# Kernel tuning notes

Hardware: AMD Instinct MI355X
Metric: run time of the kernel (lower is better)

The kernel has to match this reference:

```python
import jax, jax.numpy as jnp
import numpy as np

TOP_K = 3
EPS = 1e-12  # F.normalize eps


def _lstm(x, W_ih, W_hh, b_ih, b_hh):
    # x: [B, S, I]; PyTorch gate order i, f, g, o; returns h sequence [B, S, H]
    B = x.shape[0]
    H = W_hh.shape[1]
    xs = jnp.swapaxes(x, 0, 1)  # [S, B, I]
    x_proj = xs @ W_ih.T + b_ih + b_hh  # [S, B, 4H]

    def step(carry, xp):
        h, c = carry
        gates = xp + h @ W_hh.T
        i, f, g, o = jnp.split(gates, 4, axis=-1)
        i = jax.nn.sigmoid(i); f = jax.nn.sigmoid(f)
        g = jnp.tanh(g); o = jax.nn.sigmoid(o)
        c = f * c + i * g
        h = o * jnp.tanh(c)
        return (h, c), h

    init = (jnp.zeros((B, H), x.dtype), jnp.zeros((B, H), x.dtype))
    _, hs = jax.lax.scan(step, init, x_proj)
    return jnp.swapaxes(hs, 0, 1)  # [B, S, H]


def setup_inputs() -> dict:
    key = jax.random.key(0)
    ks = jax.random.split(key, 16)
    B, S, I, H, M, N, O = 4, 256, 512, 1024, 256, 65536, 512
    sc = 0.02
    return {
        "x": jax.random.normal(ks[0], (B, S, I), jnp.float32),
        "keys": jax.random.normal(ks[1], (N, M), jnp.float32),
        "values": jax.random.normal(ks[2], (N, M), jnp.float32),
        "importance": jnp.ones((N,), jnp.float32),
        "W_ih": jax.random.normal(ks[3], (4 * H, I), jnp.float32) * sc,
        "W_hh": jax.random.normal(ks[4], (4 * H, H), jnp.float32) * sc,
        "b_ih": jnp.zeros((4 * H,), jnp.float32),
        "b_hh": jnp.zeros((4 * H,), jnp.float32),
        "Wq": jax.random.normal(ks[5], (M, H), jnp.float32) * sc,
        "bq": jnp.zeros((M,), jnp.float32),
        "Wa": jax.random.normal(ks[6], (1, M), jnp.float32) * sc,
        "ba": jnp.zeros((1,), jnp.float32),
        "Wc": jax.random.normal(ks[7], (M, M), jnp.float32) * sc,
        "bc": jnp.zeros((M,), jnp.float32),
        "Wo": jax.random.normal(ks[8], (O, H + M), jnp.float32) * sc,
        "bo": jnp.zeros((O,), jnp.float32),
    }


def reference(x, keys, values, importance, W_ih, W_hh, b_ih, b_hh,
              Wq, bq, Wa, ba, Wc, bc, Wo, bo):
    # Controller LSTM over the whole sequence
    h = _lstm(x, W_ih, W_hh, b_ih, b_hh)  # [B, S, H]

    # Query projection and cosine similarity against the memory keys
    q = h @ Wq.T + bq  # [B, S, M]
    qn = q / jnp.maximum(jnp.linalg.norm(q, axis=-1, keepdims=True), EPS)
    kn = keys / jnp.maximum(jnp.linalg.norm(keys, axis=-1, keepdims=True), EPS)
    sim = jnp.einsum("bsm,nm->bsn", qn, kn) * importance  # [B, S, N]

    # Top-k retrieval and value gather
    _, top_idx = jax.lax.top_k(sim, TOP_K)  # [B, S, k]
    retrieved = values[top_idx]  # [B, S, k, M]

    # Learned attention over retrieved memories
    att_logits = (retrieved @ Wa.T + ba)[..., 0]  # [B, S, k]
    att = jax.nn.softmax(att_logits, axis=-1)
    mem = jnp.einsum("bsk,bskm->bsm", att, retrieved)
    mem = mem @ Wc.T + bc  # combine_layer

    out = jnp.concatenate([h, mem], axis=-1) @ Wo.T + bo  # [B, S, O]
    return out
```

## Files before the change

kernel.cpp:

```cpp
#include <hip/hip_runtime.h>
#include <hip/hip_bf16.h>
#include <cstdint>
#include <cstddef>

#define BB 4
#define SS 256
#define ID 512
#define HD 1024
#define MD 256
#define NKEY 65536
#define OD 512
#define ROWS 1024
#define NWG_LSTM 256
#define NTH_LSTM 256
#define KPB 2048
#define KSPLITS (NKEY / KPB)

typedef __attribute__((ext_vector_type(8))) short bf16x8;
typedef __attribute__((ext_vector_type(4))) float f32x4;
typedef __attribute__((ext_vector_type(8))) unsigned short u16x8;

__global__ __launch_bounds__(256) void sgemm_nt(
    const float* __restrict__ A, int lda,
    const float* __restrict__ Bm, int ldb,
    float* __restrict__ C, int ldc, int K,
    const float* __restrict__ bias, const float* __restrict__ bias2,
    int accum)
{
    __shared__ float As[64][17];
    __shared__ float Bs[64][17];
    const int t = threadIdx.x;
    const int tx = t & 15, ty = t >> 4;
    const int bm = blockIdx.y << 6, bn = blockIdx.x << 6;
    const int lrow = t >> 2, lk4 = (t & 3) << 2;
    float acc[4][4] = {};

    for (int kb = 0; kb < K; kb += 16) {
        const float4 av = *(const float4*)&A[(size_t)(bm + lrow) * lda + kb + lk4];
        const float4 bv = *(const float4*)&Bm[(size_t)(bn + lrow) * ldb + kb + lk4];
        __syncthreads();
        As[lrow][lk4 + 0] = av.x; As[lrow][lk4 + 1] = av.y;
        As[lrow][lk4 + 2] = av.z; As[lrow][lk4 + 3] = av.w;
        Bs[lrow][lk4 + 0] = bv.x; Bs[lrow][lk4 + 1] = bv.y;
        Bs[lrow][lk4 + 2] = bv.z; Bs[lrow][lk4 + 3] = bv.w;
        __syncthreads();
#pragma unroll
        for (int k = 0; k < 16; ++k) {
            const float a0 = As[4 * ty + 0][k], a1 = As[4 * ty + 1][k];
            const float a2 = As[4 * ty + 2][k], a3 = As[4 * ty + 3][k];
            const float b0 = Bs[4 * tx + 0][k], b1 = Bs[4 * tx + 1][k];
            const float b2 = Bs[4 * tx + 2][k], b3 = Bs[4 * tx + 3][k];
            acc[0][0] += a0 * b0; acc[0][1] += a0 * b1; acc[0][2] += a0 * b2; acc[0][3] += a0 * b3;
            acc[1][0] += a1 * b0; acc[1][1] += a1 * b1; acc[1][2] += a1 * b2; acc[1][3] += a1 * b3;
            acc[2][0] += a2 * b0; acc[2][1] += a2 * b1; acc[2][2] += a2 * b2; acc[2][3] += a2 * b3;
            acc[3][0] += a3 * b0; acc[3][1] += a3 * b1; acc[3][2] += a3 * b2; acc[3][3] += a3 * b3;
        }
    }

#pragma unroll
    for (int i = 0; i < 4; ++i) {
        const int row = bm + 4 * ty + i;
        const int col = bn + 4 * tx;
        float4* cp = (float4*)&C[(size_t)row * ldc + col];
        float4 r;
        if (accum) {
            const float4 old = *cp;
            r.x = old.x + acc[i][0]; r.y = old.y + acc[i][1];
            r.z = old.z + acc[i][2]; r.w = old.w + acc[i][3];
        } else {
            float bx = bias[col + 0], by = bias[col + 1], bz = bias[col + 2], bw = bias[col + 3];
            if (bias2) { bx += bias2[col + 0]; by += bias2[col + 1]; bz += bias2[col + 2]; bw += bias2[col + 3]; }
            r.x = acc[i][0] + bx; r.y = acc[i][1] + by;
            r.z = acc[i][2] + bz; r.w = acc[i][3] + bw;
        }
        *cp = r;
    }
}

__global__ void rownorm(const float* __restrict__ X, const float* __restrict__ imp,
                        float* __restrict__ scale_out, float* __restrict__ Xn, int nrows)
{
    const int row = blockIdx.x * 4 + (threadIdx.x >> 6);
    const int lane = threadIdx.x & 63;
    if (row >= nrows) return;
    float4 v = *(const float4*)&X[(size_t)row * 256 + (lane << 2)];
    float ss = v.x * v.x + v.y * v.y + v.z * v.z + v.w * v.w;
#pragma unroll
    for (int o = 1; o < 64; o <<= 1) ss += __shfl_xor(ss, o);
    float sc = 1.f / fmaxf(sqrtf(ss), 1e-12f);
    if (imp) sc *= imp[row];
    if (scale_out && lane == 0) scale_out[row] = sc;
    if (Xn) {
        v.x *= sc; v.y *= sc; v.z *= sc; v.w *= sc;
        *(float4*)&Xn[(size_t)row * 256 + (lane << 2)] = v;
    }
}

__device__ inline float sigm_f(float x) { return 1.f / (1.f + __expf(-x)); }
__device__ inline float tanh_f(float x) { return 1.f - 2.f / (__expf(2.f * x) + 1.f); }

#define SUBSTEP(B, U, UN, C4, XPC) do {                                           \
    asm volatile("s_waitcnt vmcnt(3)" ::: "memory");                              \
    __builtin_amdgcn_sched_barrier(0);                                            \
    const unsigned* pb_ = rec + (slot << 12) + (B << 10) + (t << 2);              \
    while ((((U.x ^ st) | (U.y ^ st) | (U.z ^ st) | (U.w ^ st)) & 0xFFu) != 0u) { \
        __builtin_amdgcn_s_sleep(1);                                              \
        asm volatile("global_load_dwordx4 %0, %1, off sc0 sc1\n\ts_waitcnt vmcnt(0)" \
                     : "=&v"(U) : "v"(pb_) : "memory");                           \
    }                                                                             \
    {                                                                             \
        float4 hw_;                                                               \
        hw_.x = __uint_as_float(U.x & 0xFFFFFF00u);                               \
        hw_.y = __uint_as_float(U.y & 0xFFFFFF00u);                               \
        hw_.z = __uint_as_float(U.z & 0xFFFFFF00u);                               \
        hw_.w = __uint_as_float(U.w & 0xFFFFFF00u);                               \
        *(float4*)&h_lds[B][t << 2] = hw_;                                        \
    }                                                                             \
    asm volatile("s_waitcnt lgkmcnt(0)" ::: "memory");                            \
    __builtin_amdgcn_sched_barrier(0);                                            \
    __builtin_amdgcn_s_barrier();                                                 \
    {                                                                             \
        const unsigned* pn_ = rec + (((B == 3) ? (slot ^ 1) : slot) << 12)        \
                              + (((B + 1) & 3) << 10) + (t << 2);                 \
        asm volatile("global_load_dwordx4 %0, %1, off sc0 sc1"                    \
                     : "=&v"(UN) : "v"(pn_) : "memory");                          \
    }                                                                             \
    const float* hb_ = &h_lds[B][0];                                              \
    float ax_ = 0.f, ay_ = 0.f, az_ = 0.f, aw_ = 0.f;                             \
    _Pragma("unroll")                                                             \
    for (int j = 0; j < 16; ++j) {                                                \
        const float4 hv_ = *(const float4*)&hb_[(ksub << 2) + (j << 6)];          \
        ax_ += w4[j].x * hv_.x; ay_ += w4[j].y * hv_.y;                           \
        az_ += w4[j].z * hv_.z; aw_ += w4[j].w * hv_.w;                           \
    }                                                                             \
    float sm_ = (ax_ + ay_) + (az_ + aw_);                                        \
    sm_ += __shfl_xor(sm_, 1); sm_ += __shfl_xor(sm_, 2);                         \
    sm_ += __shfl_xor(sm_, 4); sm_ += __shfl_xor(sm_, 8);                         \
    sm_ += XPC;                                                                   \
    const float vi_ = __shfl(sm_, ksub);                                          \
    const float vf_ = __shfl(sm_, ksub + 16);                                     \
    const float vg_ = __shfl(sm_, ksub + 32);                                     \
    const float vo_ = __shfl(sm_, ksub + 48);                                     \
    const float iv_ = sigm_f(vi_), fv_ = sigm_f(vf_);                             \
    const float gv_ = tanh_f(vg_), ov_ = sigm_f(vo_);                             \
    C4 = fv_ * C4 + iv_ * gv_;                                                    \
    const float hvv_ = ov_ * tanh_f(C4);                                          \
    if (lane == 0) {                                                              \
        unsigned* dst_ = rec + ((slot ^ 1) << 12) + (B << 10) + unit;             \
        const unsigned uv_ = (__float_as_uint(hvv_) & 0xFFFFFF00u) |              \
                             ((unsigned)(s + 1) & 0xFFu);                         \
        float* ha_ = &h_all[(size_t)((B << 8) + s) * 1024 + unit];                \
        asm volatile("global_store_dword %0, %1, off sc0 sc1"                     \
                     :: "v"(dst_), "v"(uv_) : "memory");                          \
        asm volatile("global_store_dword %0, %1, off"                             \
                     :: "v"(ha_), "v"(hvv_) : "memory");                          \
    }                                                                             \
    {                                                                             \
        const float* px_ = &xp[(size_t)((B << 8) + sn) * 4096 + wrow];            \
        asm volatile("global_load_dword %0, %1, off"                              \
                     : "=&v"(XPC) : "v"(px_) : "memory");                         \
    }                                                                             \
} while (0)

__global__ __launch_bounds__(256) void lstm_kernel(
    const float* __restrict__ xp, const float* __restrict__ W_hh,
    unsigned* __restrict__ rec, float* __restrict__ h_all)
{
    __shared__ float h_lds[4][1024];
    const int t = threadIdx.x;
    const int wave = t >> 6, lane = t & 63;
    const int gt = lane >> 4, ksub = lane & 15;
    const int unit = (blockIdx.x << 2) + wave;
    const int wrow = (gt << 10) + unit;

    float4 w4[16];
#pragma unroll
    for (int j = 0; j < 16; ++j)
        w4[j] = *(const float4*)&W_hh[(size_t)wrow * 1024 + (ksub << 2) + (j << 6)];

    float c40 = 0.f, c41 = 0.f, c42 = 0.f, c43 = 0.f;
    float xpc0 = xp[(size_t)(0 * 256 + 0) * 4096 + wrow];
    float xpc1 = xp[(size_t)(1 * 256 + 0) * 4096 + wrow];
    float xpc2 = xp[(size_t)(2 * 256 + 0) * 4096 + wrow];
    float xpc3 = xp[(size_t)(3 * 256 + 0) * 4096 + wrow];

    uint4 u0 = make_uint4(~0u, ~0u, ~0u, ~0u);
    uint4 u1 = u0, u2 = u0, u3 = u0;

    {
        const unsigned* p00 = rec + (t << 2);
        asm volatile("global_load_dwordx4 %0, %1, off sc0 sc1\n\ts_waitcnt vmcnt(0)"
                     : "=&v"(u0) : "v"(p00) : "memory");
        __builtin_amdgcn_sched_barrier(0);
    }

    for (int s = 0; s < 256; ++s) {
        const int slot = s & 1;
        const unsigned st = (unsigned)s & 0xFFu;
        const int sn = (s < 255) ? s + 1 : 255;
        SUBSTEP(0, u0, u1, c40, xpc0);
        SUBSTEP(1, u1, u2, c41, xpc1);
        SUBSTEP(2, u2, u3, c42, xpc2);
        SUBSTEP(3, u3, u0, c43, xpc3);
    }
}

#define SWAP1(A, B, IA, IB) { float _t = A; A = B; B = _t; int _u = IA; IA = IB; IB = _u; }
#define INS8G(P, V, ID) do {                                          \
    const float _v = (V); const int _id = (ID);                       \
    if (_v > P##v7) {                                                 \
        P##v7 = _v; P##i7 = _id;                                      \
        if (P##v7 > P##v6) SWAP1(P##v6, P##v7, P##i6, P##i7);         \
        if (P##v6 > P##v5) SWAP1(P##v5, P##v6, P##i5, P##i6);         \
        if (P##v5 > P##v4) SWAP1(P##v4, P##v5, P##i4, P##i5);         \
        if (P##v4 > P##v3) SWAP1(P##v3, P##v4, P##i3, P##i4);         \
        if (P##v3 > P##v2) SWAP1(P##v2, P##v3, P##i2, P##i3);         \
        if (P##v2 > P##v1) SWAP1(P##v1, P##v2, P##i1, P##i2);         \
        if (P##v1 > P##v0) SWAP1(P##v0, P##v1, P##i0, P##i1);         \
    }                                                                 \
} while (0)
#define DECL8(P) float P##v0=-3e38f,P##v1=-3e38f,P##v2=-3e38f,P##v3=-3e38f, \
                       P##v4=-3e38f,P##v5=-3e38f,P##v6=-3e38f,P##v7=-3e38f; \
                 int P##i0=0x7fffffff,P##i1=0x7fffffff,P##i2=0x7fffffff,P##i3=0x7fffffff, \
                     P##i4=0x7fffffff,P##i5=0x7fffffff,P##i6=0x7fffffff,P##i7=0x7fffffff;

__device__ inline unsigned pack_bf16(float a, float b) {
    return (__float_as_uint(a) >> 16) | (__float_as_uint(b) & 0xFFFF0000u);
}

__global__ __launch_bounds__(256) void sim_mfma(
    const float* __restrict__ qn, const float* __restrict__ keys,
    const float* __restrict__ rnk, float* __restrict__ part_v8, int* __restrict__ part_i8)
{
    __shared__ unsigned short k_lds[64 * 264];
    __shared__ float cand_v[256 * 8];
    __shared__ int   cand_i[256 * 8];
    const int t = threadIdx.x;
    const int wave = t >> 6, lane = t & 63;
    const int ks = blockIdx.x, qs = blockIdx.y;
    const int key_base = ks * KPB;
    const int q0 = qs << 6;
    const int qrow = q0 + (wave << 4) + (lane & 15);
    const int kg = lane >> 4;

    bf16x8 bq[8];
#pragma unroll
    for (int kc = 0; kc < 8; ++kc) {
        const float* qp = &qn[(size_t)qrow * 256 + (kc << 5) + (kg << 3)];
        const float4 f0 = *(const float4*)qp;
        const float4 f1 = *(const float4*)(qp + 4);
        union { unsigned int u[4]; bf16x8 h; } cv;
        cv.u[0] = pack_bf16(f0.x, f0.y);
        cv.u[1] = pack_bf16(f0.z, f0.w);
        cv.u[2] = pack_bf16(f1.x, f1.y);
        cv.u[3] = pack_bf16(f1.z, f1.w);
        bq[kc] = cv.h;
    }

    DECL8(t)

    for (int stg = 0; stg < KPB / 64; ++stg) {
        __syncthreads();
#pragma unroll
        for (int i = 0; i < 8; ++i) {
            const int g = (i << 11) + (t << 3);
            const int row = g >> 8, col = g & 255;
            const int krow = key_base + (stg << 6) + row;
            const float sc = rnk[krow];
            const float* kp = &keys[(size_t)krow * 256 + col];
            float4 f0 = *(const float4*)kp;
            float4 f1 = *(const float4*)(kp + 4);
            f0.x *= sc; f0.y *= sc; f0.z *= sc; f0.w *= sc;
            f1.x *= sc; f1.y *= sc; f1.z *= sc; f1.w *= sc;
            union { unsigned int u[4]; u16x8 h; } cv;
            cv.u[0] = pack_bf16(f0.x, f0.y);
            cv.u[1] = pack_bf16(f0.z, f0.w);
            cv.u[2] = pack_bf16(f1.x, f1.y);
            cv.u[3] = pack_bf16(f1.z, f1.w);
            *(u16x8*)&k_lds[row * 264 + col] = cv.h;
        }
        __syncthreads();

#pragma unroll
        for (int kt = 0; kt < 4; ++kt) {
            f32x4 a0 = {0.f, 0.f, 0.f, 0.f};
            f32x4 a1 = {0.f, 0.f, 0.f, 0.f};
#pragma unroll
            for (int kc = 0; kc < 4; ++kc) {
                const bf16x8 af = *(const bf16x8*)&k_lds[((kt << 4) + (lane & 15)) * 264 +
                                                         (kc << 5) + (kg << 3)];
                a0 = __builtin_amdgcn_mfma_f32_16x16x32_bf16(af, bq[kc], a0, 0, 0, 0);
            }
#pragma unroll
            for (int kc = 4; kc < 8; ++kc) {
                const bf16x8 af = *(const bf16x8*)&k_lds[((kt << 4) + (lane & 15)) * 264 +
                                                         (kc << 5) + (kg << 3)];
                a1 = __builtin_amdgcn_mfma_f32_16x16x32_bf16(af, bq[kc], a1, 0, 0, 0);
            }
            const int kidx = key_base + (stg << 6) + (kt << 4) + (kg << 2);
            INS8G(t, a0[0] + a1[0], kidx + 0);
            INS8G(t, a0[1] + a1[1], kidx + 1);
            INS8G(t, a0[2] + a1[2], kidx + 2);
            INS8G(t, a0[3] + a1[3], kidx + 3);
        }
    }

    __syncthreads();
    cand_v[t * 8 + 0] = tv0; cand_i[t * 8 + 0] = ti0;
    cand_v[t * 8 + 1] = tv1; cand_i[t * 8 + 1] = ti1;
    cand_v[t * 8 + 2] = tv2; cand_i[t * 8 + 2] = ti2;
    cand_v[t * 8 + 3] = tv3; cand_i[t * 8 + 3] = ti3;
    cand_v[t * 8 + 4] = tv4; cand_i[t * 8 + 4] = ti4;
    cand_v[t * 8 + 5] = tv5; cand_i[t * 8 + 5] = ti5;
    cand_v[t * 8 + 6] = tv6; cand_i[t * 8 + 6] = ti6;
    cand_v[t * 8 + 7] = tv7; cand_i[t * 8 + 7] = ti7;
    __syncthreads();
    if (t < 64) {
        DECL8(m)
        const int w = t >> 4, c = t & 15;
        for (int g = 0; g < 4; ++g) {
            const int src = ((w << 6) + c + (g << 4)) * 8;
            for (int r = 0; r < 8; ++r)
                INS8G(m, cand_v[src + r], cand_i[src + r]);
        }
        const size_t base = (size_t)(q0 + t) * (KSPLITS * 8) + ks * 8;
        part_v8[base + 0] = mv0; part_i8[base + 0] = mi0;
        part_v8[base + 1] = mv1; part_i8[base + 1] = mi1;
        part_v8[base + 2] = mv2; part_i8[base + 2] = mi2;
        part_v8[base + 3] = mv3; part_i8[base + 3] = mi3;
        part_v8[base + 4] = mv4; part_i8[base + 4] = mi4;
        part_v8[base + 5] = mv5; part_i8[base + 5] = mi5;
        part_v8[base + 6] = mv6; part_i8[base + 6] = mi6;
        part_v8[base + 7] = mv7; part_i8[base + 7] = mi7;
    }
}

__global__ void cand_merge(const float* __restrict__ part_v8, const int* __restrict__ part_i8,
                           int* __restrict__ cand8_i)
{
    const int q = blockIdx.x * 256 + threadIdx.x;
    if (q >= ROWS) return;
    DECL8(c)
    for (int j = 0; j < KSPLITS * 8; ++j)
        INS8G(c, part_v8[(size_t)q * (KSPLITS * 8) + j], part_i8[(size_t)q * (KSPLITS * 8) + j]);
    cand8_i[q * 8 + 0] = ci0; cand8_i[q * 8 + 1] = ci1;
    cand8_i[q * 8 + 2] = ci2; cand8_i[q * 8 + 3] = ci3;
    cand8_i[q * 8 + 4] = ci4; cand8_i[q * 8 + 5] = ci5;
    cand8_i[q * 8 + 6] = ci6; cand8_i[q * 8 + 7] = ci7;
}

__global__ void rescore(const float* __restrict__ qn, const float* __restrict__ keys,
                        const float* __restrict__ rnk, const int* __restrict__ cand8_i,
                        int* __restrict__ top_i)
{
    const int q = blockIdx.x;
    const int lane = threadIdx.x;
    const float4 qv = *(const float4*)&qn[(size_t)q * 256 + (lane << 2)];
    float s0, s1, s2, s3, s4, s5, s6, s7;
    int j0, j1, j2, j3, j4, j5, j6, j7;
#define RES(R, S, J) { J = cand8_i[q * 8 + R]; \
    const float4 kv = *(const float4*)&keys[(size_t)J * 256 + (lane << 2)]; \
    float d = qv.x * kv.x + qv.y * kv.y + qv.z * kv.z + qv.w * kv.w; \
    d += __shfl_xor(d, 1); d += __shfl_xor(d, 2); d += __shfl_xor(d, 4); \
    d += __shfl_xor(d, 8); d += __shfl_xor(d, 16); d += __shfl_xor(d, 32); \
    S = d * rnk[J]; }
    RES(0, s0, j0) RES(1, s1, j1) RES(2, s2, j2) RES(3, s3, j3)
    RES(4, s4, j4) RES(5, s5, j5) RES(6, s6, j6) RES(7, s7, j7)
#undef RES
    if (lane == 0) {
#define BET(SV, JV) if (SV > bv || (SV == bv && JV < bi)) { bv = SV; bi = JV; }
#pragma unroll
        for (int k = 0; k < 3; ++k) {
            float bv = s0; int bi = j0;
            BET(s1, j1) BET(s2, j2) BET(s3, j3) BET(s4, j4)
            BET(s5, j5) BET(s6, j6) BET(s7, j7)
            top_i[q * 3 + k] = bi;
            if (j0 == bi) s0 = -3e38f;
            if (j1 == bi) s1 = -3e38f;
            if (j2 == bi) s2 = -3e38f;
            if (j3 == bi) s3 = -3e38f;
            if (j4 == bi) s4 = -3e38f;
            if (j5 == bi) s5 = -3e38f;
            if (j6 == bi) s6 = -3e38f;
            if (j7 == bi) s7 = -3e38f;
        }
#undef BET
    }
}

__global__ void mem_gather(const int* __restrict__ top_i, const float* __restrict__ values,
                           const float* __restrict__ Wa, const float* __restrict__ ba,
                           float* __restrict__ mem_raw)
{
    const int q = blockIdx.x;
    const int lane = threadIdx.x;
    const float4 wa = *(const float4*)&Wa[lane << 2];
    float4 vr[3];
    float lg[3];
#pragma unroll
    for (int r = 0; r < 3; ++r) {
        const int n = top_i[q * 3 + r];
        const float4 v = *(const float4*)&values[(size_t)n * 256 + (lane << 2)];
        vr[r] = v;
        float d = v.x * wa.x + v.y * wa.y + v.z * wa.z + v.w * wa.w;
#pragma unroll
        for (int o = 1; o < 64; o <<= 1) d += __shfl_xor(d, o);
        lg[r] = d + ba[0];
    }
    const float mx = fmaxf(lg[0], fmaxf(lg[1], lg[2]));
    float e0 = __expf(lg[0] - mx), e1 = __expf(lg[1] - mx), e2 = __expf(lg[2] - mx);
    const float inv = 1.f / (e0 + e1 + e2);
    e0 *= inv; e1 *= inv; e2 *= inv;
    float4 m;
    m.x = e0 * vr[0].x + e1 * vr[1].x + e2 * vr[2].x;
    m.y = e0 * vr[0].y + e1 * vr[1].y + e2 * vr[2].y;
    m.z = e0 * vr[0].z + e1 * vr[1].z + e2 * vr[2].z;
    m.w = e0 * vr[0].w + e1 * vr[1].w + e2 * vr[2].w;
    *(float4*)&mem_raw[(size_t)q * 256 + (lane << 2)] = m;
}

extern "C" void kernel_launch(void* const* d_in, const int* in_sizes, int n_in,
                              void* d_out, int out_size, void* d_ws, size_t ws_size,
                              hipStream_t stream)
{
    (void)in_sizes; (void)n_in; (void)out_size; (void)ws_size;
    const float* x     = (const float*)d_in[0];
    const float* keys  = (const float*)d_in[1];
    const float* values= (const float*)d_in[2];
    const float* imp   = (const float*)d_in[3];
    const float* W_ih  = (const float*)d_in[4];
    const float* W_hh  = (const float*)d_in[5];
    const float* b_ih  = (const float*)d_in[6];
    const float* b_hh  = (const float*)d_in[7];
    const float* Wq    = (const float*)d_in[8];
    const float* bq    = (const float*)d_in[9];
    const float* Wa    = (const float*)d_in[10];
    const float* ba    = (const float*)d_in[11];
    const float* Wc    = (const float*)d_in[12];
    const float* bc    = (const float*)d_in[13];
    const float* Wo    = (const float*)d_in[14];
    const float* bo    = (const float*)d_in[15];
    float* out = (float*)d_out;

    float* ws = (float*)d_ws;
    size_t o = 0;
    float* xp      = ws + o; o += (size_t)1024 * 4096;
    float* h_all   = ws + o; o += (size_t)1024 * 1024;
    unsigned* rec  = (unsigned*)(ws + o); o += 2 * 4096;
    float* rnk     = ws + o; o += NKEY;
    float* qbuf    = ws + o; o += (size_t)ROWS * 256;
    float* qn      = ws + o; o += (size_t)ROWS * 256;
    float* part_v8 = ws + o; o += (size_t)ROWS * KSPLITS * 8;
    int*   part_i8 = (int*)(ws + o); o += (size_t)ROWS * KSPLITS * 8;
    int*   cand8_i = (int*)(ws + o); o += ROWS * 8;
    int*   top_i   = (int*)(ws + o); o += 4096;
    float* mem_raw = ws + o; o += (size_t)ROWS * 256;
    float* memb    = ws + o; o += (size_t)ROWS * 256;

    hipMemsetAsync(rec, 0, 2 * 4096 * 4, stream);

    rownorm<<<NKEY / 4, 256, 0, stream>>>(keys, imp, rnk, nullptr, NKEY);

    sgemm_nt<<<dim3(64, 16), 256, 0, stream>>>(x, ID, W_ih, ID, xp, 4096, ID, b_ih, b_hh, 0);

    lstm_kernel<<<NWG_LSTM, NTH_LSTM, 0, stream>>>(xp, W_hh, rec, h_all);

    sgemm_nt<<<dim3(4, 16), 256, 0, stream>>>(h_all, HD, Wq, HD, qbuf, MD, HD, bq, nullptr, 0);

    rownorm<<<ROWS / 4, 256, 0, stream>>>(qbuf, nullptr, nullptr, qn, ROWS);

    sim_mfma<<<dim3(KSPLITS, 16), 256, 0, stream>>>(qn, keys, rnk, part_v8, part_i8);
    cand_merge<<<ROWS / 256, 256, 0, stream>>>(part_v8, part_i8, cand8_i);
    rescore<<<ROWS, 64, 0, stream>>>(qn, keys, rnk, cand8_i, top_i);

    mem_gather<<<ROWS, 64, 0, stream>>>(top_i, values, Wa, ba, mem_raw);

    sgemm_nt<<<dim3(4, 16), 256, 0, stream>>>(mem_raw, MD, Wc, MD, memb, MD, MD, bc, nullptr, 0);

    sgemm_nt<<<dim3(8, 16), 256, 0, stream>>>(h_all, HD, Wo, HD + MD, out, OD, HD, bo, nullptr, 0);
    sgemm_nt<<<dim3(8, 16), 256, 0, stream>>>(memb, MD, Wo + HD, HD + MD, out, OD, MD, nullptr, nullptr, 1);
}
```

Before: 1.377 ms.

## Pre-normalize keys to bf16 once, widen input-projection GEMM tile, fuse rescore with gather

The key-normalization pass now also writes a bf16 copy of the scaled keys into workspace, so the similarity kernel stages half the bytes per tile and skips the per-tile fp32 scaling and conversion. It falls back to the old fp32 path if the workspace is too small. The input-projection GEMM gets a specialized 64x128-tile kernel with hard-coded dimensions. The rescore and value-gather kernels are merged into one launch, removing the top-index round trip. The cost is an extra 32 MB bf16 write in the keys pass, and every query-tile block still re-reads the bf16 keys.

```diff
diff --git a/kernel.cpp b/kernel.cpp
--- a/kernel.cpp
+++ b/kernel.cpp
@@ -77,8 +77,72 @@
     }
 }
 
+__global__ __launch_bounds__(256) void sgemm_nt_w(
+    const float* __restrict__ A, const float* __restrict__ Bm,
+    float* __restrict__ C, const float* __restrict__ bias, const float* __restrict__ bias2)
+{
+    __shared__ float As[16][64];
+    __shared__ float Bs[16][128];
+    const int t = threadIdx.x;
+    const int tx = t & 15, ty = t >> 4;
+    const int bm = blockIdx.y << 6, bn = blockIdx.x << 7;
+    const int arow = t & 63, akq = t >> 6;
+    const int brow = t & 127, bkq = t >> 7;
+    float acc[4][8] = {};
+
+    for (int kb = 0; kb < 512; kb += 16) {
+        const float4 av  = *(const float4*)&A[(size_t)(bm + arow) * 512 + kb + (akq << 2)];
+        const float4 bv0 = *(const float4*)&Bm[(size_t)(bn + brow) * 512 + kb + (bkq << 3)];
+        const float4 bv1 = *(const float4*)&Bm[(size_t)(bn + brow) * 512 + kb + (bkq << 3) + 4];
+        __syncthreads();
+        As[(akq << 2) + 0][arow] = av.x; As[(akq << 2) + 1][arow] = av.y;
+        As[(akq << 2) + 2][arow] = av.z; As[(akq << 2) + 3][arow] = av.w;
+        Bs[(bkq << 3) + 0][brow] = bv0.x; Bs[(bkq << 3) + 1][brow] = bv0.y;
+        Bs[(bkq << 3) + 2][brow] = bv0.z; Bs[(bkq << 3) + 3][brow] = bv0.w;
+        Bs[(bkq << 3) + 4][brow] = bv1.x; Bs[(bkq << 3) + 5][brow] = bv1.y;
+        Bs[(bkq << 3) + 6][brow] = bv1.z; Bs[(bkq << 3) + 7][brow] = bv1.w;
+        __syncthreads();
+#pragma unroll
+        for (int k = 0; k < 16; ++k) {
+            const float4 a  = *(const float4*)&As[k][ty << 2];
+            const float4 b0 = *(const float4*)&Bs[k][tx << 3];
+            const float4 b1 = *(const float4*)&Bs[k][(tx << 3) + 4];
+            acc[0][0] += a.x * b0.x; acc[0][1] += a.x * b0.y; acc[0][2] += a.x * b0.z; acc[0][3] += a.x * b0.w;
+            acc[0][4] += a.x * b1.x; acc[0][5] += a.x * b1.y; acc[0][6] += a.x * b1.z; acc[0][7] += a.x * b1.w;
+            acc[1][0] += a.y * b0.x; acc[1][1] += a.y * b0.y; acc[1][2] += a.y * b0.z; acc[1][3] += a.y * b0.w;
+            acc[1][4] += a.y * b1.x; acc[1][5] += a.y * b1.y; acc[1][6] += a.y * b1.z; acc[1][7] += a.y * b1.w;
+            acc[2][0] += a.z * b0.x; acc[2][1] += a.z * b0.y; acc[2][2] += a.z * b0.z; acc[2][3] += a.z * b0.w;
+            acc[2][4] += a.z * b1.x; acc[2][5] += a.z * b1.y; acc[2][6] += a.z * b1.z; acc[2][7] += a.z * b1.w;
+            acc[3][0] += a.w * b0.x; acc[3][1] += a.w * b0.y; acc[3][2] += a.w * b0.z; acc[3][3] += a.w * b0.w;
+            acc[3][4] += a.w * b1.x; acc[3][5] += a.w * b1.y; acc[3][6] += a.w * b1.z; acc[3][7] += a.w * b1.w;
+        }
+    }
+
+#pragma unroll
+    for (int i = 0; i < 4; ++i) {
+        const int row = bm + (ty << 2) + i;
+        const int col = bn + (tx << 3);
+        float4 r0, r1;
+        r0.x = acc[i][0] + bias[col + 0] + bias2[col + 0];
+        r0.y = acc[i][1] + bias[col + 1] + bias2[col + 1];
+        r0.z = acc[i][2] + bias[col + 2] + bias2[col + 2];
+        r0.w = acc[i][3] + bias[col + 3] + bias2[col + 3];
+        r1.x = acc[i][4] + bias[col + 4] + bias2[col + 4];
+        r1.y = acc[i][5] + bias[col + 5] + bias2[col + 5];
+        r1.z = acc[i][6] + bias[col + 6] + bias2[col + 6];
+        r1.w = acc[i][7] + bias[col + 7] + bias2[col + 7];
+        *(float4*)&C[(size_t)row * 4096 + col] = r0;
+        *(float4*)&C[(size_t)row * 4096 + col + 4] = r1;
+    }
+}
+
+__device__ inline unsigned pack_bf16(float a, float b) {
+    return (__float_as_uint(a) >> 16) | (__float_as_uint(b) & 0xFFFF0000u);
+}
+
 __global__ void rownorm(const float* __restrict__ X, const float* __restrict__ imp,
-                        float* __restrict__ scale_out, float* __restrict__ Xn, int nrows)
+                        float* __restrict__ scale_out, float* __restrict__ Xn,
+                        unsigned short* __restrict__ kb, int nrows)
 {
     const int row = blockIdx.x * 4 + (threadIdx.x >> 6);
     const int lane = threadIdx.x & 63;
@@ -93,6 +157,12 @@
     if (Xn) {
         v.x *= sc; v.y *= sc; v.z *= sc; v.w *= sc;
         *(float4*)&Xn[(size_t)row * 256 + (lane << 2)] = v;
+    }
+    if (kb) {
+        uint2 p;
+        p.x = pack_bf16(v.x * sc, v.y * sc);
+        p.y = pack_bf16(v.z * sc, v.w * sc);
+        *(uint2*)&kb[(size_t)row * 256 + (lane << 2)] = p;
     }
 }
 
@@ -224,13 +294,9 @@
                  int P##i0=0x7fffffff,P##i1=0x7fffffff,P##i2=0x7fffffff,P##i3=0x7fffffff, \
                      P##i4=0x7fffffff,P##i5=0x7fffffff,P##i6=0x7fffffff,P##i7=0x7fffffff;
 
-__device__ inline unsigned pack_bf16(float a, float b) {
-    return (__float_as_uint(a) >> 16) | (__float_as_uint(b) & 0xFFFF0000u);
-}
-
-__global__ __launch_bounds__(256) void sim_mfma(
-    const float* __restrict__ qn, const float* __restrict__ keys,
-    const float* __restrict__ rnk, float* __restrict__ part_v8, int* __restrict__ part_i8)
+__global__ __launch_bounds__(256) void sim_mfma_b(
+    const float* __restrict__ qn, const unsigned short* __restrict__ kb,
+    float* __restrict__ part_v8, int* __restrict__ part_i8)
 {
     __shared__ unsigned short k_lds[64 * 264];
     __shared__ float cand_v[256 * 8];
@@ -259,25 +325,15 @@
 
     DECL8(t)
 
+    const int srow = t >> 2, scol0 = (t & 3) << 6;
+
     for (int stg = 0; stg < KPB / 64; ++stg) {
         __syncthreads();
-#pragma unroll
-        for (int i = 0; i < 8; ++i) {
-            const int g = (i << 11) + (t << 3);
-            const int row = g >> 8, col = g & 255;
-            const int krow = key_base + (stg << 6) + row;
-            const float sc = rnk[krow];
-            const float* kp = &keys[(size_t)krow * 256 + col];
-            float4 f0 = *(const float4*)kp;
-            float4 f1 = *(const float4*)(kp + 4);
-            f0.x *= sc; f0.y *= sc; f0.z *= sc; f0.w *= sc;
-            f1.x *= sc; f1.y *= sc; f1.z *= sc; f1.w *= sc;
-            union { unsigned int u[4]; u16x8 h; } cv;
-            cv.u[0] = pack_bf16(f0.x, f0.y);
-            cv.u[1] = pack_bf16(f0.z, f0.w);
-            cv.u[2] = pack_bf16(f1.x, f1.y);
-            cv.u[3] = pack_bf16(f1.z, f1.w);
-            *(u16x8*)&k_lds[row * 264 + col] = cv.h;
+        {
+            const unsigned short* kp = &kb[(size_t)(key_base + (stg << 6) + srow) * 256 + scol0];
+#pragma unroll
+            for (int i = 0; i < 8; ++i)
+                *(u16x8*)&k_lds[srow * 264 + scol0 + (i << 3)] = *(const u16x8*)(kp + (i << 3));
         }
         __syncthreads();
 
@@ -335,6 +391,113 @@
     }
 }
 
+__global__ __launch_bounds__(256) void sim_mfma_f(
+    const float* __restrict__ qn, const float* __restrict__ keys,
+    const float* __restrict__ rnk, float* __restrict__ part_v8, int* __restrict__ part_i8)
+{
+    __shared__ unsigned short k_lds[64 * 264];
+    __shared__ float cand_v[256 * 8];
+    __shared__ int   cand_i[256 * 8];
+    const int t = threadIdx.x;
+    const int wave = t >> 6, lane = t & 63;
+    const int ks = blockIdx.x, qs = blockIdx.y;
+    const int key_base = ks * KPB;
+    const int q0 = qs << 6;
+    const int qrow = q0 + (wave << 4) + (lane & 15);
+    const int kg = lane >> 4;
+
+    bf16x8 bq[8];
+#pragma unroll
+    for (int kc = 0; kc < 8; ++kc) {
+        const float* qp = &qn[(size_t)qrow * 256 + (kc << 5) + (kg << 3)];
+        const float4 f0 = *(const float4*)qp;
+        const float4 f1 = *(const float4*)(qp + 4);
+        union { unsigned int u[4]; bf16x8 h; } cv;
+        cv.u[0] = pack_bf16(f0.x, f0.y);
+        cv.u[1] = pack_bf16(f0.z, f0.w);
+        cv.u[2] = pack_bf16(f1.x, f1.y);
+        cv.u[3] = pack_bf16(f1.z, f1.w);
+        bq[kc] = cv.h;
+    }
+
+    DECL8(t)
+
+    for (int stg = 0; stg < KPB / 64; ++stg) {
+        __syncthreads();
+#pragma unroll
+        for (int i = 0; i < 8; ++i) {
+            const int g = (i << 11) + (t << 3);
+            const int row = g >> 8, col = g & 255;
+            const int krow = key_base + (stg << 6) + row;
+            const float sc = rnk[krow];
+            const float* kp = &keys[(size_t)krow * 256 + col];
+            float4 f0 = *(const float4*)kp;
+            float4 f1 = *(const float4*)(kp + 4);
+            f0.x *= sc; f0.y *= sc; f0.z *= sc; f0.w *= sc;
+            f1.x *= sc; f1.y *= sc; f1.z *= sc; f1.w *= sc;
+            union { unsigned int u[4]; u16x8 h; } cv;
+            cv.u[0] = pack_bf16(f0.x, f0.y);
+            cv.u[1] = pack_bf16(f0.z, f0.w);
+            cv.u[2] = pack_bf16(f1.x, f1.y);
+            cv.u[3] = pack_bf16(f1.z, f1.w);
+            *(u16x8*)&k_lds[row * 264 + col] = cv.h;
+        }
+        __syncthreads();
+
+#pragma unroll
+        for (int kt = 0; kt < 4; ++kt) {
+            f32x4 a0 = {0.f, 0.f, 0.f, 0.f};
+            f32x4 a1 = {0.f, 0.f, 0.f, 0.f};
+#pragma unroll
+            for (int kc = 0; kc < 4; ++kc) {
+                const bf16x8 af = *(const bf16x8*)&k_lds[((kt << 4) + (lane & 15)) * 264 +
+                                                         (kc << 5) + (kg << 3)];
+                a0 = __builtin_amdgcn_mfma_f32_16x16x32_bf16(af, bq[kc], a0, 0, 0, 0);
+            }
+#pragma unroll
+            for (int kc = 4; kc < 8; ++kc) {
+                const bf16x8 af = *(const bf16x8*)&k_lds[((kt << 4) + (lane & 15)) * 264 +
+                                                         (kc << 5) + (kg << 3)];
+                a1 = __builtin_amdgcn_mfma_f32_16x16x32_bf16(af, bq[kc], a1, 0, 0, 0);
+            }
+            const int kidx = key_base + (stg << 6) + (kt << 4) + (kg << 2);
+            INS8G(t, a0[0] + a1[0], kidx + 0);
+            INS8G(t, a0[1] + a1[1], kidx + 1);
+            INS8G(t, a0[2] + a1[2], kidx + 2);
+            INS8G(t, a0[3] + a1[3], kidx + 3);
+        }
+    }
+
+    __syncthreads();
+    cand_v[t * 8 + 0] = tv0; cand_i[t * 8 + 0] = ti0;
+    cand_v[t * 8 + 1] = tv1; cand_i[t * 8 + 1] = ti1;
+    cand_v[t * 8 + 2] = tv2; cand_i[t * 8 + 2] = ti2;
+    cand_v[t * 8 + 3] = tv3; cand_i[t * 8 + 3] = ti3;
+    cand_v[t * 8 + 4] = tv4; cand_i[t * 8 + 4] = ti4;
+    cand_v[t * 8 + 5] = tv5; cand_i[t * 8 + 5] = ti5;
+    cand_v[t * 8 + 6] = tv6; cand_i[t * 8 + 6] = ti6;
+    cand_v[t * 8 + 7] = tv7; cand_i[t * 8 + 7] = ti7;
+    __syncthreads();
+    if (t < 64) {
+        DECL8(m)
+        const int w = t >> 4, c = t & 15;
+        for (int g = 0; g < 4; ++g) {
+            const int src = ((w << 6) + c + (g << 4)) * 8;
+            for (int r = 0; r < 8; ++r)
+                INS8G(m, cand_v[src + r], cand_i[src + r]);
+        }
+        const size_t base = (size_t)(q0 + t) * (KSPLITS * 8) + ks * 8;
+        part_v8[base + 0] = mv0; part_i8[base + 0] = mi0;
+        part_v8[base + 1] = mv1; part_i8[base + 1] = mi1;
+        part_v8[base + 2] = mv2; part_i8[base + 2] = mi2;
+        part_v8[base + 3] = mv3; part_i8[base + 3] = mi3;
+        part_v8[base + 4] = mv4; part_i8[base + 4] = mi4;
+        part_v8[base + 5] = mv5; part_i8[base + 5] = mi5;
+        part_v8[base + 6] = mv6; part_i8[base + 6] = mi6;
+        part_v8[base + 7] = mv7; part_i8[base + 7] = mi7;
+    }
+}
+
 __global__ void cand_merge(const float* __restrict__ part_v8, const int* __restrict__ part_i8,
                            int* __restrict__ cand8_i)
 {
@@ -349,9 +512,10 @@
     cand8_i[q * 8 + 6] = ci6; cand8_i[q * 8 + 7] = ci7;
 }
 
-__global__ void rescore(const float* __restrict__ qn, const float* __restrict__ keys,
-                        const float* __restrict__ rnk, const int* __restrict__ cand8_i,
-                        int* __restrict__ top_i)
+__global__ void rescore_gather(const float* __restrict__ qn, const float* __restrict__ keys,
+                               const float* __restrict__ rnk, const int* __restrict__ cand8_i,
+                               const float* __restrict__ values, const float* __restrict__ Wa,
+                               const float* __restrict__ ba, float* __restrict__ mem_raw)
 {
     const int q = blockIdx.x;
     const int lane = threadIdx.x;
@@ -367,40 +531,30 @@
     RES(0, s0, j0) RES(1, s1, j1) RES(2, s2, j2) RES(3, s3, j3)
     RES(4, s4, j4) RES(5, s5, j5) RES(6, s6, j6) RES(7, s7, j7)
 #undef RES
-    if (lane == 0) {
+    int top[3];
 #define BET(SV, JV) if (SV > bv || (SV == bv && JV < bi)) { bv = SV; bi = JV; }
 #pragma unroll
-        for (int k = 0; k < 3; ++k) {
-            float bv = s0; int bi = j0;
-            BET(s1, j1) BET(s2, j2) BET(s3, j3) BET(s4, j4)
-            BET(s5, j5) BET(s6, j6) BET(s7, j7)
-            top_i[q * 3 + k] = bi;
-            if (j0 == bi) s0 = -3e38f;
-            if (j1 == bi) s1 = -3e38f;
-            if (j2 == bi) s2 = -3e38f;
-            if (j3 == bi) s3 = -3e38f;
-            if (j4 == bi) s4 = -3e38f;
-            if (j5 == bi) s5 = -3e38f;
-            if (j6 == bi) s6 = -3e38f;
-            if (j7 == bi) s7 = -3e38f;
-        }
+    for (int k = 0; k < 3; ++k) {
+        float bv = s0; int bi = j0;
+        BET(s1, j1) BET(s2, j2) BET(s3, j3) BET(s4, j4)
+        BET(s5, j5) BET(s6, j6) BET(s7, j7)
+        top[k] = bi;
+        if (j0 == bi) s0 = -3e38f;
+        if (j1 == bi) s1 = -3e38f;
+        if (j2 == bi) s2 = -3e38f;
+        if (j3 == bi) s3 = -3e38f;
+        if (j4 == bi) s4 = -3e38f;
+        if (j5 == bi) s5 = -3e38f;
+        if (j6 == bi) s6 = -3e38f;
+        if (j7 == bi) s7 = -3e38f;
+    }
 #undef BET
-    }
-}
-
-__global__ void mem_gather(const int* __restrict__ top_i, const float* __restrict__ values,
-                           const float* __restrict__ Wa, const float* __restrict__ ba,
-                           float* __restrict__ mem_raw)
-{
-    const int q = blockIdx.x;
-    const int lane = threadIdx.x;
     const float4 wa = *(const float4*)&Wa[lane << 2];
     float4 vr[3];
     float lg[3];
 #pragma unroll
     for (int r = 0; r < 3; ++r) {
-        const int n = top_i[q * 3 + r];
-        const float4 v = *(const float4*)&values[(size_t)n * 256 + (lane << 2)];
+        const float4 v = *(const float4*)&values[(size_t)top[r] * 256 + (lane << 2)];
         vr[r] = v;
         float d = v.x * wa.x + v.y * wa.y + v.z * wa.z + v.w * wa.w;
 #pragma unroll
@@ -423,7 +577,7 @@
                               void* d_out, int out_size, void* d_ws, size_t ws_size,
                               hipStream_t stream)
 {
-    (void)in_sizes; (void)n_in; (void)out_size; (void)ws_size;
+    (void)in_sizes; (void)n_in; (void)out_size;
     const float* x     = (const float*)d_in[0];
     const float* keys  = (const float*)d_in[1];
     const float* values= (const float*)d_in[2];
@@ -453,27 +607,31 @@
     float* part_v8 = ws + o; o += (size_t)ROWS * KSPLITS * 8;
     int*   part_i8 = (int*)(ws + o); o += (size_t)ROWS * KSPLITS * 8;
     int*   cand8_i = (int*)(ws + o); o += ROWS * 8;
-    int*   top_i   = (int*)(ws + o); o += 4096;
     float* mem_raw = ws + o; o += (size_t)ROWS * 256;
     float* memb    = ws + o; o += (size_t)ROWS * 256;
+    unsigned short* kb = (unsigned short*)(ws + o);
+    const size_t need_bf16 = (o + (size_t)NKEY * 256 / 2) * sizeof(float);
+    const bool use_bf16 = ws_size >= need_bf16;
 
     hipMemsetAsync(rec, 0, 2 * 4096 * 4, stream);
 
-    rownorm<<<NKEY / 4, 256, 0, stream>>>(keys, imp, rnk, nullptr, NKEY);
-
-    sgemm_nt<<<dim3(64, 16), 256, 0, stream>>>(x, ID, W_ih, ID, xp, 4096, ID, b_ih, b_hh, 0);
+    rownorm<<<NKEY / 4, 256, 0, stream>>>(keys, imp, rnk, nullptr,
+                                          use_bf16 ? kb : nullptr, NKEY);
+
+    sgemm_nt_w<<<dim3(32, 16), 256, 0, stream>>>(x, W_ih, xp, b_ih, b_hh);
 
     lstm_kernel<<<NWG_LSTM, NTH_LSTM, 0, stream>>>(xp, W_hh, rec, h_all);
 
     sgemm_nt<<<dim3(4, 16), 256, 0, stream>>>(h_all, HD, Wq, HD, qbuf, MD, HD, bq, nullptr, 0);
 
-    rownorm<<<ROWS / 4, 256, 0, stream>>>(qbuf, nullptr, nullptr, qn, ROWS);
-
-    sim_mfma<<<dim3(KSPLITS, 16), 256, 0, stream>>>(qn, keys, rnk, part_v8, part_i8);
+    rownorm<<<ROWS / 4, 256, 0, stream>>>(qbuf, nullptr, nullptr, qn, nullptr, ROWS);
+
+    if (use_bf16)
+        sim_mfma_b<<<dim3(KSPLITS, 16), 256, 0, stream>>>(qn, kb, part_v8, part_i8);
+    else
+        sim_mfma_f<<<dim3(KSPLITS, 16), 256, 0, stream>>>(qn, keys, rnk, part_v8, part_i8);
     cand_merge<<<ROWS / 256, 256, 0, stream>>>(part_v8, part_i8, cand8_i);
-    rescore<<<ROWS, 64, 0, stream>>>(qn, keys, rnk, cand8_i, top_i);
-
-    mem_gather<<<ROWS, 64, 0, stream>>>(top_i, values, Wa, ba, mem_raw);
+    rescore_gather<<<ROWS, 64, 0, stream>>>(qn, keys, rnk, cand8_i, values, Wa, ba, mem_raw);
 
     sgemm_nt<<<dim3(4, 16), 256, 0, stream>>>(mem_raw, MD, Wc, MD, memb, MD, MD, bc, nullptr, 0);
 
```

Result: faster. 1.344 ms (-2.4%).
